# Optimization experiments

Hardware: AMD Instinct MI355X
Metric: run time of the kernel (lower is better)

The kernel has to match this reference:

```python
import jax, jax.numpy as jnp
import numpy as np

NEG = jnp.float32(-1e9)  # -inf surrogate, safe for logsumexp
EPS = 1e-7               # keras.backend.epsilon()


def _ctc_loss(y_true, y_pred):
    """Faithful K.ctc_batch_cost with full input/label lengths.

    y_true: [B, L] int labels in [0, C-2] (blank = C-1, TF convention)
    y_pred: [B, T, C] softmax probabilities
    returns: [B, 1] negative log-likelihood per sample
    """
    B, T, C = y_pred.shape
    L = y_true.shape[1]
    blank = C - 1
    S = 2 * L + 1  # extended label: blank-interleaved

    logp = jnp.log(y_pred + EPS)  # [B, T, C]

    # Extended label sequence [blank, l1, blank, l2, ..., lL, blank]
    ext = jnp.full((B, S), blank, dtype=jnp.int32).at[:, 1::2].set(
        y_true.astype(jnp.int32))  # [B, S]

    # Skip transition (s-2 -> s) allowed iff ext[s] != blank and ext[s] != ext[s-2]
    skip = jnp.concatenate(
        [jnp.zeros((B, 2), dtype=bool),
         (ext[:, 2:] != blank) & (ext[:, 2:] != ext[:, :-2])],
        axis=1)  # [B, S]

    # Gather lattice log-probs once: [B, T, S]
    lp = jnp.take_along_axis(logp, ext[:, None, :], axis=2)

    # alpha at t=0: only states 0 (blank) and 1 (first label) reachable
    alpha0 = jnp.full((B, S), NEG).at[:, 0].set(lp[:, 0, 0]).at[:, 1].set(lp[:, 0, 1])

    def step(alpha, lp_t):
        a1 = alpha                                                     # stay
        a2 = jnp.pad(alpha[:, :-1], ((0, 0), (1, 0)), constant_values=NEG)  # advance 1
        a3 = jnp.pad(alpha[:, :-2], ((0, 0), (2, 0)), constant_values=NEG)  # advance 2
        a3 = jnp.where(skip, a3, NEG)
        new = lp_t + jax.nn.logsumexp(jnp.stack([a1, a2, a3]), axis=0)
        return new, None

    lp_rest = jnp.transpose(lp[:, 1:, :], (1, 0, 2))  # [T-1, B, S]
    alphaT, _ = jax.lax.scan(step, alpha0, lp_rest)

    # Total log-prob ends in last blank or last label
    ll = jax.nn.logsumexp(alphaT[:, S - 2:S], axis=1)  # [B]
    return -ll[:, None]  # [B, 1], matches ctc_batch_cost's expand_dims


def setup_inputs() -> dict:
    key = jax.random.key(0)
    k1, k2 = jax.random.split(key)
    B, T, C, L = 512, 512, 128, 64
    logits = jax.random.normal(k1, (B, T, C), dtype=jnp.float32)
    y_pred = jax.nn.softmax(logits, axis=-1)  # ctc_batch_cost expects probs
    y_true = jax.random.randint(k2, (B, L), 0, C - 1)  # labels exclude blank C-1
    return {"y_true": y_true, "y_pred": y_pred}


def reference(y_true, y_pred):
    return _ctc_loss(y_true, y_pred)
```

## Files before the change

kernel.cpp:

```cpp
#include <hip/hip_runtime.h>
#include <stdint.h>


constexpr float EPSF = 1e-7f;
constexpr float LN2F = 0.6931471805599453f;

template<int CTRL>
__device__ __forceinline__ float dpp_mov(float x) {
    return __int_as_float(__builtin_amdgcn_update_dpp(
        0, __float_as_int(x), CTRL, 0xF, 0xF, true));
}

__device__ __forceinline__ void gload_lds16(const void* g, void* l) {
    __builtin_amdgcn_global_load_lds(
        (const __attribute__((address_space(1))) void*)g,
        (__attribute__((address_space(3))) void*)l, 16, 0, 0);
}

__global__ __launch_bounds__(64)
void ctc_fwd(const int* __restrict__ y_true,
             const float* __restrict__ y_pred,
             float* __restrict__ out)
{
    __shared__ float lds[2][64][128];

    const int b    = blockIdx.x;
    const int lane = threadIdx.x;

    const char* __restrict__ gbase =
        (const char*)(y_pred + (size_t)b * 512 * 128);

    const int   lab   = y_true[b * 64 + lane];
    const int   labp  = __shfl_up(lab, 1, 64);
    const float skipf = (lane > 0 && lab != labp) ? 1.0f : 0.0f;
    const bool  l0    = (lane == 0);

    {
        const char* g = gbase + lane * 16;
        #pragma unroll
        for (int j = 0; j < 32; ++j)
            gload_lds16(g + j * 1024, (char*)&lds[0][0][0] + j * 1024);
    }

    float aZ = 0.0f, aA = 0.0f, aB = 0.0f;
    int   shift = 0;
    float red   = 0.0f;

    #pragma unroll 1
    for (int c = 0; c < 8; ++c) {
        if (c < 7) {
            const char* g = gbase + (size_t)(c + 1) * 32768 + lane * 16;
            char*       l = (char*)&lds[(c + 1) & 1][0][0];
            #pragma unroll
            for (int j = 0; j < 32; ++j)
                gload_lds16(g + j * 1024, l + j * 1024);
            asm volatile("s_waitcnt vmcnt(32)" ::: "memory");
        } else {
            asm volatile("s_waitcnt vmcnt(0)" ::: "memory");
        }

        const float* ch = &lds[c & 1][0][0];

        float vB = ch[lane * 128 + 127] + EPSF;

        float ring[8];
        #pragma unroll
        for (int j = 0; j < 8; ++j) ring[j] = ch[j * 128 + lab];

        #pragma unroll
        for (int u = 0; u < 64; ++u) {
            float pl = ring[u & 7] + EPSF;
            float pb = __int_as_float(
                __builtin_amdgcn_readlane(__float_as_int(vB), u));

            if (c == 0 && u == 0) {
                aZ = pb;
                aA = l0 ? pl : 0.0f;
                aB = 0.0f;
            } else {
                float upA = dpp_mov<0x138>(aA);
                float upB = dpp_mov<0x138>(aB);
                upB = l0 ? aZ : upB;
                float ts = aA + upB;
                ts = fmaf(skipf, upA, ts);
                float nA = pl * ts;
                float nB = pb * (aB + aA);
                aZ *= pb;
                aA = nA; aB = nB;
            }

            if ((u & 7) == 3) {
                float r = fmaxf(fmaxf(aA, aB), aZ);
                r = fmaxf(r, dpp_mov<0x111>(r));
                r = fmaxf(r, dpp_mov<0x112>(r));
                r = fmaxf(r, dpp_mov<0x114>(r));
                r = fmaxf(r, dpp_mov<0x118>(r));
                r = fmaxf(r, dpp_mov<0x142>(r));
                r = fmaxf(r, dpp_mov<0x143>(r));
                red = r;
            }
            if ((u & 7) == 7) {
                int mb = __builtin_amdgcn_readlane(__float_as_int(red), 63);
                int e  = (mb >> 23) & 0xff;
                int f  = 314 - e;
                f = f < 1 ? 1 : (f > 254 ? 254 : f);
                float scale = __int_as_float(f << 23);
                shift += f - 127;
                aA *= scale; aB *= scale; aZ *= scale;
            }

            if (u < 56)
                ring[u & 7] = ch[(u + 8) * 128 + lab];
        }
    }

    float s   = aA + aB;
    float ll2 = __builtin_amdgcn_logf(s);
    if (lane == 63) out[b] = ((float)shift - ll2) * LN2F;
}

extern "C" void kernel_launch(void* const* d_in, const int* in_sizes, int n_in,
                              void* d_out, int out_size, void* d_ws, size_t ws_size,
                              hipStream_t stream)
{
    const int*   y_true = (const int*)d_in[0];
    const float* y_pred = (const float*)d_in[1];
    float*       out    = (float*)d_out;

    const int B = out_size;
    ctc_fwd<<<dim3(B), dim3(64), 0, stream>>>(y_true, y_pred, out);
}
```

Baseline: 193.5 us.

## Deepen LDS prefetch pipeline to four 32-timestep buffers

Splits the per-block y_pred stream into 16 chunks of 32 timesteps and keeps a four-slot LDS ring with three chunks in flight, instead of two 64-timestep double buffers. Prefetch for chunk c+3 is issued after waiting on chunk c, so global loads stay further ahead of the serial recurrence. It also folds the epsilon add into the ring load. LDS use stays the same, but the outer loop runs twice as many iterations, each with its own wait and issue overhead.

After: 193.3 us. About the same (-0.1%).

```diff
diff --git a/kernel.cpp b/kernel.cpp
--- a/kernel.cpp
+++ b/kernel.cpp
@@ -22,7 +22,7 @@
              const float* __restrict__ y_pred,
              float* __restrict__ out)
 {
-    __shared__ float lds[2][64][128];
+    __shared__ float lds[4][32][128];
 
     const int b    = blockIdx.x;
     const int lane = threadIdx.x;
@@ -34,12 +34,15 @@
     const int   labp  = __shfl_up(lab, 1, 64);
     const float skipf = (lane > 0 && lab != labp) ? 1.0f : 0.0f;
     const bool  l0    = (lane == 0);
+    const int   rlane = lane & 31;
 
-    {
-        const char* g = gbase + lane * 16;
+    #pragma unroll
+    for (int k = 0; k < 3; ++k) {
+        const char* g = gbase + k * 16384 + lane * 16;
+        char*       l = (char*)&lds[k][0][0];
         #pragma unroll
-        for (int j = 0; j < 32; ++j)
-            gload_lds16(g + j * 1024, (char*)&lds[0][0][0] + j * 1024);
+        for (int j = 0; j < 16; ++j)
+            gload_lds16(g + j * 1024, l + j * 1024);
     }
 
     float aZ = 0.0f, aA = 0.0f, aB = 0.0f;
@@ -47,33 +50,36 @@
     float red   = 0.0f;
 
     #pragma unroll 1
-    for (int c = 0; c < 8; ++c) {
-        if (c < 7) {
-            const char* g = gbase + (size_t)(c + 1) * 32768 + lane * 16;
-            char*       l = (char*)&lds[(c + 1) & 1][0][0];
+    for (int c = 0; c < 16; ++c) {
+        if (c <= 13)      asm volatile("s_waitcnt vmcnt(32)" ::: "memory");
+        else if (c == 14) asm volatile("s_waitcnt vmcnt(16)" ::: "memory");
+        else              asm volatile("s_waitcnt vmcnt(0)"  ::: "memory");
+
+        if (c + 3 < 16) {
+            const char* g = gbase + (c + 3) * 16384 + lane * 16;
+            char*       l = (char*)&lds[(c + 3) & 3][0][0];
             #pragma unroll
-            for (int j = 0; j < 32; ++j)
+            for (int j = 0; j < 16; ++j)
                 gload_lds16(g + j * 1024, l + j * 1024);
-            asm volatile("s_waitcnt vmcnt(32)" ::: "memory");
-        } else {
-            asm volatile("s_waitcnt vmcnt(0)" ::: "memory");
         }
 
-        const float* ch = &lds[c & 1][0][0];
+        const float* ch = &lds[c & 3][0][0];
 
-        float vB = ch[lane * 128 + 127] + EPSF;
+        float vB = ch[rlane * 128 + 127] + EPSF;
 
         float ring[8];
         #pragma unroll
-        for (int j = 0; j < 8; ++j) ring[j] = ch[j * 128 + lab];
+        for (int j = 0; j < 8; ++j) ring[j] = ch[j * 128 + lab] + EPSF;
+
+        const bool first = (c == 0);
 
         #pragma unroll
-        for (int u = 0; u < 64; ++u) {
-            float pl = ring[u & 7] + EPSF;
+        for (int u = 0; u < 32; ++u) {
+            float pl = ring[u & 7];
             float pb = __int_as_float(
                 __builtin_amdgcn_readlane(__float_as_int(vB), u));
 
-            if (c == 0 && u == 0) {
+            if (u == 0 && first) {
                 aZ = pb;
                 aA = l0 ? pl : 0.0f;
                 aB = 0.0f;
@@ -109,8 +115,8 @@
                 aA *= scale; aB *= scale; aZ *= scale;
             }
 
-            if (u < 56)
-                ring[u & 7] = ch[(u + 8) * 128 + lab];
+            if (u < 24)
+                ring[u & 7] = ch[(u + 8) * 128 + lab] + EPSF;
         }
     }
 
```
